# Optimization experiments

Hardware: AMD Instinct MI355X
Metric: run time of the kernel (lower is better)

Reference implementation:

```python
import jax, jax.numpy as jnp
import numpy as np

B, T = 64, 256
STOCH, DETER = 1024, 4096
D = 512          # attention_dim == embed_dim == heads*dim_head
H, HD = 8, 64    # heads, dim_head
FF = 2 * D       # feedforward hidden
L = 2            # transformer layers
NT = 255         # embedding rows (len(targets))
OUT = 255        # np.prod(shape)
SCALE = HD ** -0.5
EPS = 1e-5


def _ln(x, g, b):
    m = jnp.mean(x, axis=-1, keepdims=True)
    v = jnp.mean((x - m) ** 2, axis=-1, keepdims=True)
    return (x - m) * jax.lax.rsqrt(v + EPS) * g + b


def setup_inputs() -> dict:
    key = jax.random.key(0)
    ks = jax.random.split(key, 32)
    r = lambda i, shp, s=0.02: (jax.random.normal(ks[i], shp, dtype=jnp.float32) * s)
    inp = {
        'stoch': jax.random.normal(ks[0], (B, T, STOCH), dtype=jnp.float32),
        'deter': jax.random.normal(ks[1], (B, T, DETER), dtype=jnp.float32),
        'targets_array': jax.random.randint(ks[2], (B, T), 0, NT),
        'emb': r(3, (NT, D), 1.0),
        'Ws': r(4, (D, STOCH)), 'bs': jnp.zeros((D,), jnp.float32),
        'Wd': r(5, (D, DETER)), 'bd': jnp.zeros((D,), jnp.float32),
        # per-layer stacked params [L, ...]
        'ln1_g': jnp.ones((L, D), jnp.float32), 'ln1_b': jnp.zeros((L, D), jnp.float32),
        'Wqkv': r(6, (L, 3 * H * HD, D)),
        'Wout': r(7, (L, D, H * HD)), 'bout': jnp.zeros((L, D), jnp.float32),
        'ln2_g': jnp.ones((L, D), jnp.float32), 'ln2_b': jnp.zeros((L, D), jnp.float32),
        'W1': r(8, (L, FF, D)), 'b1': jnp.zeros((L, FF), jnp.float32),
        'W2': r(9, (L, D, FF)), 'b2': jnp.zeros((L, D), jnp.float32),
        'W1b': r(10, (L, FF, D)), 'b1b': jnp.zeros((L, FF), jnp.float32),
        'W2b': r(11, (L, D, FF)), 'b2b': jnp.zeros((L, D), jnp.float32),
        'Wm': r(12, (OUT, D)), 'bm': jnp.zeros((OUT,), jnp.float32),
    }
    return inp


def _forward(stoch, deter, targets_array, emb, Ws, bs, Wd, bd,
             ln1_g, ln1_b, Wqkv, Wout, bout, ln2_g, ln2_b,
             W1, b1, W2, b2, W1b, b1b, W2b, b2b, Wm, bm):
    N = B * T
    s = stoch.reshape(N, STOCH)
    d = deter.reshape(N, DETER)
    tg = targets_array.reshape(N)
    tok1 = (s @ Ws.T + bs)[:, None, :]   # [N,1,D]
    tok2 = (d @ Wd.T + bd)[:, None, :]
    x = jnp.concatenate([tok1, tok2], axis=1)   # [N,2,D]
    q2 = emb[tg][:, None, :]                    # [N,1,D]

    for l in range(L):
        # PreNorm -> Attention (residuals connect to the normalized inputs,
        # exactly as in the original code)
        xn = _ln(x, ln1_g[l], ln1_b[l])
        qn = _ln(q2, ln1_g[l], ln1_b[l])
        qkv = xn @ Wqkv[l].T                            # [N,2,3*H*HD]
        q, k, v = jnp.split(qkv, 3, axis=-1)
        q = q.reshape(N, 2, H, HD).transpose(0, 2, 1, 3)   # [N,H,2,HD]
        k = k.reshape(N, 2, H, HD).transpose(0, 2, 1, 3)
        v = v.reshape(N, 2, H, HD).transpose(0, 2, 1, 3)
        qq2 = qn.reshape(N, 1, H, HD).transpose(0, 2, 1, 3)  # [N,H,1,HD]
        dots = jnp.einsum('nhqd,nhkd->nhqk', q, k) * SCALE
        dots2 = jnp.einsum('nhqd,nhkd->nhqk', qq2, k) * SCALE
        attn = jax.nn.log_softmax(dots, axis=-1)    # LogSoftmax attention!
        attn2 = jax.nn.log_softmax(dots2, axis=-1)
        out = jnp.einsum('nhqk,nhkd->nhqd', attn, v).transpose(0, 2, 1, 3).reshape(N, 2, H * HD)
        qout = jnp.einsum('nhqk,nhkd->nhqd', attn2, v).transpose(0, 2, 1, 3).reshape(N, 1, H * HD)
        x = out @ Wout[l].T + bout[l] + xn   # to_out on self stream only
        q2 = qout + qn                        # cross stream has NO projection

        # PreNorm -> FeedForward (dual streams, separate MLPs, exact GELU)
        xn = _ln(x, ln2_g[l], ln2_b[l])
        qn = _ln(q2, ln2_g[l], ln2_b[l])
        x = jax.nn.gelu(xn @ W1[l].T + b1[l], approximate=False) @ W2[l].T + b2[l] + xn
        q2 = jax.nn.gelu(qn @ W1b[l].T + b1b[l], approximate=False) @ W2b[l].T + b2b[l] + qn

    out = q2.reshape(B, T, D)
    mean = out @ Wm.T + bm   # [B,T,OUT]
    return mean


def reference(stoch, deter, targets_array, emb, Ws, bs, Wd, bd,
              ln1_g, ln1_b, Wqkv, Wout, bout, ln2_g, ln2_b,
              W1, b1, W2, b2, W1b, b1b, W2b, b2b, Wm, bm):
    return _forward(stoch, deter, targets_array, emb, Ws, bs, Wd, bd,
                    ln1_g, ln1_b, Wqkv, Wout, bout, ln2_g, ln2_b,
                    W1, b1, W2, b2, W1b, b1b, W2b, b2b, Wm, bm)
```

## Files before the change

kernel.cpp:

```cpp
#include <hip/hip_runtime.h>
#include <cstdint>
#include <cstddef>


#define NTOK   16384
#define TWO_N  32768
#define DMODEL 512
#define HEADS  8
#define HDIM   64
#define FFDIM  1024
#define KSTOCH 1024
#define KDETER 4096
#define QKVD   1536
#define NOUT   255

typedef short bf16x8 __attribute__((ext_vector_type(8)));
typedef float f32x4  __attribute__((ext_vector_type(4)));

__device__ inline unsigned short bfbits(float f) {
  union { float f; unsigned u; } x; x.f = f;
  unsigned r = x.u + 0x7fffu + ((x.u >> 16) & 1u);
  return (unsigned short)(r >> 16);
}
__device__ inline float bf2f(unsigned short s) {
  union { unsigned u; float f; } x; x.u = ((unsigned)s) << 16;
  return x.f;
}
__device__ inline float wave_sum(float v) {
  #pragma unroll
  for (int o = 32; o > 0; o >>= 1) v += __shfl_xor(v, o);
  return v;
}

struct CvtEnt { const float* src; unsigned short* dst; int n4; int ntot4; };
struct CvtArgs { CvtEnt e[11]; };

__global__ __launch_bounds__(256) void cvt_kernel(CvtArgs args) {
  CvtEnt ent = args.e[blockIdx.y];
  int stride = gridDim.x * 256;
  for (int i = blockIdx.x * 256 + threadIdx.x; i < ent.ntot4; i += stride) {
    float4 v;
    if (i < ent.n4) v = ((const float4*)ent.src)[i];
    else            v = make_float4(0.f, 0.f, 0.f, 0.f);
    ushort4 o;
    o.x = bfbits(v.x); o.y = bfbits(v.y); o.z = bfbits(v.z); o.w = bfbits(v.w);
    ((ushort4*)ent.dst)[i] = o;
  }
}

__global__ __launch_bounds__(128) void gather_kernel(
    const float* __restrict__ emb, const int* __restrict__ tg,
    float* __restrict__ q2) {
  int n = blockIdx.x;
  int row = tg[n];
  ((float4*)(q2 + (size_t)n * DMODEL))[threadIdx.x] =
      ((const float4*)(emb + (size_t)row * DMODEL))[threadIdx.x];
}

__global__ __launch_bounds__(256) void ln2_kernel(
    const float* __restrict__ xs, const float* __restrict__ qs,
    const float* __restrict__ g, const float* __restrict__ b,
    unsigned short* __restrict__ xb, unsigned short* __restrict__ qb) {
  int w = threadIdx.x >> 6, l = threadIdx.x & 63;
  int row = blockIdx.x * 4 + w;
  const float* src;
  unsigned short* dst;
  if (row < TWO_N) {
    src = xs + (size_t)row * DMODEL;
    dst = xb + (size_t)row * DMODEL;
  } else {
    int r2 = row - TWO_N;
    src = qs + (size_t)r2 * DMODEL;
    dst = qb + (size_t)r2 * DMODEL;
  }
  float4 v0 = ((const float4*)src)[l];
  float4 v1 = ((const float4*)src)[l + 64];
  float s  = v0.x + v0.y + v0.z + v0.w + v1.x + v1.y + v1.z + v1.w;
  float ss = v0.x*v0.x + v0.y*v0.y + v0.z*v0.z + v0.w*v0.w
           + v1.x*v1.x + v1.y*v1.y + v1.z*v1.z + v1.w*v1.w;
  s = wave_sum(s); ss = wave_sum(ss);
  float mean = s * (1.f / DMODEL);
  float var  = ss * (1.f / DMODEL) - mean * mean;
  float r = rsqrtf(var + 1e-5f);

  float4 g0 = ((const float4*)g)[l],      b0 = ((const float4*)b)[l];
  float4 g1 = ((const float4*)g)[l + 64], b1 = ((const float4*)b)[l + 64];
  ushort4 p0, p1;
  p0.x = bfbits((v0.x - mean) * r * g0.x + b0.x);
  p0.y = bfbits((v0.y - mean) * r * g0.y + b0.y);
  p0.z = bfbits((v0.z - mean) * r * g0.z + b0.z);
  p0.w = bfbits((v0.w - mean) * r * g0.w + b0.w);
  p1.x = bfbits((v1.x - mean) * r * g1.x + b1.x);
  p1.y = bfbits((v1.y - mean) * r * g1.y + b1.y);
  p1.z = bfbits((v1.z - mean) * r * g1.z + b1.z);
  p1.w = bfbits((v1.w - mean) * r * g1.w + b1.w);
  ((ushort4*)dst)[l] = p0; ((ushort4*)dst)[l + 64] = p1;
}

__global__ __launch_bounds__(256) void attn_kernel(
    const unsigned short* __restrict__ qkv, const unsigned short* __restrict__ qnb,
    float* __restrict__ q2, unsigned short* __restrict__ attnout) {
  int w = threadIdx.x >> 6, l = threadIdx.x & 63;
  int idx = blockIdx.x * 4 + w;
  int n = idx >> 3, h = idx & 7;
  const unsigned short* r0 = qkv + (size_t)(2 * n) * QKVD + h * HDIM + l;
  float q0 = bf2f(r0[0]),     k0 = bf2f(r0[512]),      v0 = bf2f(r0[1024]);
  float q1 = bf2f(r0[QKVD]),  k1 = bf2f(r0[QKVD+512]), v1 = bf2f(r0[QKVD+1024]);
  size_t qoff = (size_t)n * DMODEL + h * HDIM + l;
  float qq = bf2f(qnb[qoff]);

  float d00 = q0*k0, d01 = q0*k1, d10 = q1*k0, d11 = q1*k1, e0 = qq*k0, e1 = qq*k1;
  #pragma unroll
  for (int o = 32; o > 0; o >>= 1) {
    d00 += __shfl_xor(d00, o); d01 += __shfl_xor(d01, o);
    d10 += __shfl_xor(d10, o); d11 += __shfl_xor(d11, o);
    e0  += __shfl_xor(e0, o);  e1  += __shfl_xor(e1, o);
  }
  const float SC = 0.125f;
  d00 *= SC; d01 *= SC; d10 *= SC; d11 *= SC; e0 *= SC; e1 *= SC;
  auto lsm2 = [](float& a, float& b) {
    float m = fmaxf(a, b);
    float lse = m + logf(expf(a - m) + expf(b - m));
    a -= lse; b -= lse;
  };
  lsm2(d00, d01); lsm2(d10, d11); lsm2(e0, e1);

  float o0 = d00 * v0 + d01 * v1;
  float o1 = d10 * v0 + d11 * v1;
  float oq = e0 * v0 + e1 * v1;
  attnout[(size_t)(2 * n)     * DMODEL + h * HDIM + l] = bfbits(o0);
  attnout[(size_t)(2 * n + 1) * DMODEL + h * HDIM + l] = bfbits(o1);
  q2[qoff] = oq + qq;
}

template <bool GELU>
__global__ __launch_bounds__(256, 3) void gemm_kernel(
    const unsigned short* __restrict__ A, const unsigned short* __restrict__ B,
    const float* __restrict__ bias, const unsigned short* __restrict__ res,
    float* __restrict__ Cf, unsigned short* __restrict__ Cb,
    int M, int Nvalid, int K, int ldc, int ldcb, int ldres, int ntn) {
  __shared__ short lsA[128 * 64];
  __shared__ short lsB[128 * 64];
  int nwg = gridDim.x;
  int q8 = nwg >> 3, r8 = nwg & 7;
  int xcd = blockIdx.x & 7, lin = blockIdx.x >> 3;
  int bid = (xcd < r8 ? xcd * (q8 + 1) : r8 * (q8 + 1) + (xcd - r8) * q8) + lin;
  int tm = bid / ntn, tn = bid % ntn;
  int tid = threadIdx.x;
  int w = tid >> 6, l = tid & 63;
  int wr = w >> 1, wc = w & 1;

  int srow = w * 32 + (l >> 3);
  int scol = (l & 7) * 8;
  const unsigned short* ga = A + (size_t)(tm * 128 + srow) * K + scol;
  const unsigned short* gb = B + (size_t)(tn * 128 + srow) * K + scol;
  short* la = lsA + w * 2048;
  short* lb = lsB + w * 2048;

  f32x4 acc[4][4] = {};

  for (int k0 = 0; k0 < K; k0 += 64) {
    #pragma unroll
    for (int r = 0; r < 4; ++r) {
      __builtin_amdgcn_global_load_lds(
          (const __attribute__((address_space(1))) void*)(ga + k0 + (size_t)r * 8 * K),
          (__attribute__((address_space(3))) void*)(la + r * 512), 16, 0, 0);
      __builtin_amdgcn_global_load_lds(
          (const __attribute__((address_space(1))) void*)(gb + k0 + (size_t)r * 8 * K),
          (__attribute__((address_space(3))) void*)(lb + r * 512), 16, 0, 0);
    }
    __syncthreads();
    #pragma unroll
    for (int kk = 0; kk < 2; ++kk) {
      bf16x8 af[4], bfr[4];
      #pragma unroll
      for (int i = 0; i < 4; ++i)
        af[i] = *(const bf16x8*)(lsA + (wr * 64 + i * 16 + (l & 15)) * 64 +
                                 kk * 32 + (l >> 4) * 8);
      #pragma unroll
      for (int i = 0; i < 4; ++i)
        bfr[i] = *(const bf16x8*)(lsB + (wc * 64 + i * 16 + (l & 15)) * 64 +
                                  kk * 32 + (l >> 4) * 8);
      #pragma unroll
      for (int mi = 0; mi < 4; ++mi)
        #pragma unroll
        for (int ni = 0; ni < 4; ++ni)
          acc[mi][ni] = __builtin_amdgcn_mfma_f32_16x16x32_bf16(
              af[mi], bfr[ni], acc[mi][ni], 0, 0, 0);
    }
    __syncthreads();
  }

  int lr = l >> 4, lc = l & 15;
  #pragma unroll
  for (int mi = 0; mi < 4; ++mi) {
    #pragma unroll
    for (int ni = 0; ni < 4; ++ni) {
      int gn = tn * 128 + wc * 64 + ni * 16 + lc;
      bool okn = gn < Nvalid;
      float bv = (bias != nullptr && okn) ? bias[gn] : 0.f;
      f32x4 a = acc[mi][ni];
      #pragma unroll
      for (int j = 0; j < 4; ++j) {
        int gm = tm * 128 + wr * 64 + mi * 16 + lr * 4 + j;
        float v = a[j] + bv;
        if (GELU) v = 0.5f * v * (1.f + erff(v * 0.70710678118654752f));
        if (okn) {
          if (res) v += bf2f(res[(size_t)gm * ldres + gn]);
          if (Cf) Cf[(size_t)gm * ldc + gn] = v;
          if (Cb) Cb[(size_t)gm * ldcb + gn] = bfbits(v);
        }
      }
    }
  }
}

extern "C" void kernel_launch(void* const* d_in, const int* in_sizes, int n_in,
                              void* d_out, int out_size, void* d_ws, size_t ws_size,
                              hipStream_t stream) {
  const float* stoch = (const float*)d_in[0];
  const float* deter = (const float*)d_in[1];
  const int*   tg    = (const int*)d_in[2];
  const float* emb   = (const float*)d_in[3];
  const float* Ws    = (const float*)d_in[4];
  const float* bs    = (const float*)d_in[5];
  const float* Wd    = (const float*)d_in[6];
  const float* bd    = (const float*)d_in[7];
  const float* ln1g  = (const float*)d_in[8];
  const float* ln1b  = (const float*)d_in[9];
  const float* Wqkv  = (const float*)d_in[10];
  const float* Wout  = (const float*)d_in[11];
  const float* bout  = (const float*)d_in[12];
  const float* ln2g  = (const float*)d_in[13];
  const float* ln2b  = (const float*)d_in[14];
  const float* W1    = (const float*)d_in[15];
  const float* b1    = (const float*)d_in[16];
  const float* W2    = (const float*)d_in[17];
  const float* b2    = (const float*)d_in[18];
  const float* W1b   = (const float*)d_in[19];
  const float* b1b   = (const float*)d_in[20];
  const float* W2b   = (const float*)d_in[21];
  const float* b2b   = (const float*)d_in[22];
  const float* Wm    = (const float*)d_in[23];
  const float* bm    = (const float*)d_in[24];
  float* out = (float*)d_out;

  char* p = (char*)d_ws;
  size_t off = 0;
  auto alloc = [&](size_t bytes) {
    void* r = p + off;
    off += (bytes + 255) & ~(size_t)255;
    return r;
  };
  unsigned short* s_bf = (unsigned short*)alloc((size_t)NTOK * KSTOCH * 2);
  unsigned short* d_bf = (unsigned short*)alloc((size_t)NTOK * KDETER * 2);
  float* x    = (float*)alloc((size_t)TWO_N * DMODEL * 4);
  float* q2   = (float*)alloc((size_t)NTOK * DMODEL * 4);
  unsigned short* xnb  = (unsigned short*)alloc((size_t)TWO_N * DMODEL * 2);
  unsigned short* qnb  = (unsigned short*)alloc((size_t)NTOK * DMODEL * 2);
  unsigned short* qkvb = (unsigned short*)alloc((size_t)TWO_N * QKVD * 2);
  unsigned short* Wsb   = (unsigned short*)alloc((size_t)DMODEL * KSTOCH * 2);
  unsigned short* Wdb   = (unsigned short*)alloc((size_t)DMODEL * KDETER * 2);
  unsigned short* Wqkvb = (unsigned short*)alloc((size_t)2 * QKVD * DMODEL * 2);
  unsigned short* Woutb = (unsigned short*)alloc((size_t)2 * DMODEL * DMODEL * 2);
  unsigned short* W1bf  = (unsigned short*)alloc((size_t)2 * FFDIM * DMODEL * 2);
  unsigned short* W2bf  = (unsigned short*)alloc((size_t)2 * DMODEL * FFDIM * 2);
  unsigned short* W1bbf = (unsigned short*)alloc((size_t)2 * FFDIM * DMODEL * 2);
  unsigned short* W2bbf = (unsigned short*)alloc((size_t)2 * DMODEL * FFDIM * 2);
  unsigned short* Wmb   = (unsigned short*)alloc((size_t)256 * DMODEL * 2);
  unsigned short* attnout = s_bf;
  unsigned short* q2b     = d_bf;
  unsigned short* hb      = qkvb;
  unsigned short* hqb     = qkvb + (size_t)TWO_N * FFDIM;

  CvtArgs ca;
  ca.e[0]  = { stoch, s_bf,  NTOK * KSTOCH / 4,  NTOK * KSTOCH / 4 };
  ca.e[1]  = { deter, d_bf,  NTOK * KDETER / 4,  NTOK * KDETER / 4 };
  ca.e[2]  = { Ws,    Wsb,   DMODEL * KSTOCH / 4, DMODEL * KSTOCH / 4 };
  ca.e[3]  = { Wd,    Wdb,   DMODEL * KDETER / 4, DMODEL * KDETER / 4 };
  ca.e[4]  = { Wqkv,  Wqkvb, 2 * QKVD * DMODEL / 4, 2 * QKVD * DMODEL / 4 };
  ca.e[5]  = { Wout,  Woutb, 2 * DMODEL * DMODEL / 4, 2 * DMODEL * DMODEL / 4 };
  ca.e[6]  = { W1,    W1bf,  2 * FFDIM * DMODEL / 4, 2 * FFDIM * DMODEL / 4 };
  ca.e[7]  = { W2,    W2bf,  2 * DMODEL * FFDIM / 4, 2 * DMODEL * FFDIM / 4 };
  ca.e[8]  = { W1b,   W1bbf, 2 * FFDIM * DMODEL / 4, 2 * FFDIM * DMODEL / 4 };
  ca.e[9]  = { W2b,   W2bbf, 2 * DMODEL * FFDIM / 4, 2 * DMODEL * FFDIM / 4 };
  ca.e[10] = { Wm,    Wmb,   NOUT * DMODEL / 4,   256 * DMODEL / 4 };
  cvt_kernel<<<dim3(1024, 11), 256, 0, stream>>>(ca);

  gemm_kernel<false><<<128 * 4, 256, 0, stream>>>(
      s_bf, Wsb, bs, nullptr, x, nullptr, NTOK, DMODEL, KSTOCH, 2 * DMODEL, 0, 0, 4);
  gemm_kernel<false><<<128 * 4, 256, 0, stream>>>(
      d_bf, Wdb, bd, nullptr, x + DMODEL, nullptr, NTOK, DMODEL, KDETER, 2 * DMODEL, 0, 0, 4);

  gather_kernel<<<NTOK, 128, 0, stream>>>(emb, tg, q2);

  const int LN_GRID = (TWO_N + NTOK) / 4;
  for (int l = 0; l < 2; ++l) {
    ln2_kernel<<<LN_GRID, 256, 0, stream>>>(x, q2, ln1g + 512 * l, ln1b + 512 * l, xnb, qnb);
    gemm_kernel<false><<<256 * 12, 256, 0, stream>>>(
        xnb, Wqkvb + (size_t)l * QKVD * DMODEL, nullptr, nullptr, nullptr, qkvb,
        TWO_N, QKVD, DMODEL, 0, QKVD, 0, 12);
    attn_kernel<<<NTOK * HEADS / 4, 256, 0, stream>>>(qkvb, qnb, q2, attnout);
    gemm_kernel<false><<<256 * 4, 256, 0, stream>>>(
        attnout, Woutb + (size_t)l * DMODEL * DMODEL, bout + 512 * l, xnb, x, nullptr,
        TWO_N, DMODEL, DMODEL, DMODEL, 0, DMODEL, 4);
    ln2_kernel<<<LN_GRID, 256, 0, stream>>>(x, q2, ln2g + 512 * l, ln2b + 512 * l, xnb, qnb);
    gemm_kernel<true><<<256 * 8, 256, 0, stream>>>(
        xnb, W1bf + (size_t)l * FFDIM * DMODEL, b1 + 1024 * l, nullptr, nullptr, hb,
        TWO_N, FFDIM, DMODEL, 0, FFDIM, 0, 8);
    gemm_kernel<false><<<256 * 4, 256, 0, stream>>>(
        hb, W2bf + (size_t)l * DMODEL * FFDIM, b2 + 512 * l, xnb, x, nullptr,
        TWO_N, DMODEL, FFDIM, DMODEL, 0, DMODEL, 4);
    gemm_kernel<true><<<128 * 8, 256, 0, stream>>>(
        qnb, W1bbf + (size_t)l * FFDIM * DMODEL, b1b + 1024 * l, nullptr, nullptr, hqb,
        NTOK, FFDIM, DMODEL, 0, FFDIM, 0, 8);
    gemm_kernel<false><<<128 * 4, 256, 0, stream>>>(
        hqb, W2bbf + (size_t)l * DMODEL * FFDIM, b2b + 512 * l, qnb, q2, q2b,
        NTOK, DMODEL, FFDIM, DMODEL, DMODEL, DMODEL, 4);
  }

  gemm_kernel<false><<<128 * 2, 256, 0, stream>>>(
      q2b, Wmb, bm, nullptr, out, nullptr, NTOK, NOUT, DMODEL, NOUT, 0, 0, 2);

  (void)in_sizes; (void)n_in; (void)out_size; (void)ws_size;
}
```

Before: 1.810 ms.

## Fuse fp32-to-bf16 activation conversion into input projection GEMMs; store residual stream as bf16

Removes the separate conversion pass over the large stoch and deter activations. The input-projection GEMMs now load fp32 A tiles directly, convert them in registers and write bf16 into LDS. The self-stream residual x is also stored as bf16 instead of fp32, which halves its traffic in the layernorm and GEMM epilogues. In exchange the fused GEMMs lose the async global-to-LDS path for A and run with lower occupancy. Keeping the residual in bf16 also reduces its precision.

```diff
diff --git a/kernel.cpp b/kernel.cpp
--- a/kernel.cpp
+++ b/kernel.cpp
@@ -33,7 +33,7 @@
 }
 
 struct CvtEnt { const float* src; unsigned short* dst; int n4; int ntot4; };
-struct CvtArgs { CvtEnt e[11]; };
+struct CvtArgs { CvtEnt e[9]; };
 
 __global__ __launch_bounds__(256) void cvt_kernel(CvtArgs args) {
   CvtEnt ent = args.e[blockIdx.y];
@@ -58,43 +58,45 @@
 }
 
 __global__ __launch_bounds__(256) void ln2_kernel(
-    const float* __restrict__ xs, const float* __restrict__ qs,
+    const unsigned short* __restrict__ xs, const float* __restrict__ qs,
     const float* __restrict__ g, const float* __restrict__ b,
     unsigned short* __restrict__ xb, unsigned short* __restrict__ qb) {
   int w = threadIdx.x >> 6, l = threadIdx.x & 63;
   int row = blockIdx.x * 4 + w;
-  const float* src;
+  float e[8];
   unsigned short* dst;
   if (row < TWO_N) {
-    src = xs + (size_t)row * DMODEL;
+    const unsigned short* src = xs + (size_t)row * DMODEL;
+    bf16x8 v = ((const bf16x8*)src)[l];
+    #pragma unroll
+    for (int i = 0; i < 8; ++i) e[i] = bf2f((unsigned short)v[i]);
     dst = xb + (size_t)row * DMODEL;
   } else {
     int r2 = row - TWO_N;
-    src = qs + (size_t)r2 * DMODEL;
+    const float* src = qs + (size_t)r2 * DMODEL;
+    float4 v0 = ((const float4*)src)[2 * l];
+    float4 v1 = ((const float4*)src)[2 * l + 1];
+    e[0] = v0.x; e[1] = v0.y; e[2] = v0.z; e[3] = v0.w;
+    e[4] = v1.x; e[5] = v1.y; e[6] = v1.z; e[7] = v1.w;
     dst = qb + (size_t)r2 * DMODEL;
   }
-  float4 v0 = ((const float4*)src)[l];
-  float4 v1 = ((const float4*)src)[l + 64];
-  float s  = v0.x + v0.y + v0.z + v0.w + v1.x + v1.y + v1.z + v1.w;
-  float ss = v0.x*v0.x + v0.y*v0.y + v0.z*v0.z + v0.w*v0.w
-           + v1.x*v1.x + v1.y*v1.y + v1.z*v1.z + v1.w*v1.w;
+  float s = 0.f, ss = 0.f;
+  #pragma unroll
+  for (int i = 0; i < 8; ++i) { s += e[i]; ss += e[i] * e[i]; }
   s = wave_sum(s); ss = wave_sum(ss);
   float mean = s * (1.f / DMODEL);
   float var  = ss * (1.f / DMODEL) - mean * mean;
   float r = rsqrtf(var + 1e-5f);
 
-  float4 g0 = ((const float4*)g)[l],      b0 = ((const float4*)b)[l];
-  float4 g1 = ((const float4*)g)[l + 64], b1 = ((const float4*)b)[l + 64];
-  ushort4 p0, p1;
-  p0.x = bfbits((v0.x - mean) * r * g0.x + b0.x);
-  p0.y = bfbits((v0.y - mean) * r * g0.y + b0.y);
-  p0.z = bfbits((v0.z - mean) * r * g0.z + b0.z);
-  p0.w = bfbits((v0.w - mean) * r * g0.w + b0.w);
-  p1.x = bfbits((v1.x - mean) * r * g1.x + b1.x);
-  p1.y = bfbits((v1.y - mean) * r * g1.y + b1.y);
-  p1.z = bfbits((v1.z - mean) * r * g1.z + b1.z);
-  p1.w = bfbits((v1.w - mean) * r * g1.w + b1.w);
-  ((ushort4*)dst)[l] = p0; ((ushort4*)dst)[l + 64] = p1;
+  float4 g0 = ((const float4*)g)[2 * l], g1 = ((const float4*)g)[2 * l + 1];
+  float4 b0 = ((const float4*)b)[2 * l], b1 = ((const float4*)b)[2 * l + 1];
+  float gg[8] = {g0.x, g0.y, g0.z, g0.w, g1.x, g1.y, g1.z, g1.w};
+  float bb[8] = {b0.x, b0.y, b0.z, b0.w, b1.x, b1.y, b1.z, b1.w};
+  bf16x8 o;
+  #pragma unroll
+  for (int i = 0; i < 8; ++i)
+    o[i] = (short)bfbits((e[i] - mean) * r * gg[i] + bb[i]);
+  ((bf16x8*)dst)[l] = o;
 }
 
 __global__ __launch_bounds__(256) void attn_kernel(
@@ -133,9 +135,9 @@
   q2[qoff] = oq + qq;
 }
 
-template <bool GELU>
-__global__ __launch_bounds__(256, 3) void gemm_kernel(
-    const unsigned short* __restrict__ A, const unsigned short* __restrict__ B,
+template <bool GELU, bool AF32>
+__global__ __launch_bounds__(256, AF32 ? 2 : 3) void gemm_kernel(
+    const void* __restrict__ Av, const unsigned short* __restrict__ B,
     const float* __restrict__ bias, const unsigned short* __restrict__ res,
     float* __restrict__ Cf, unsigned short* __restrict__ Cb,
     int M, int Nvalid, int K, int ldc, int ldcb, int ldres, int ntn) {
@@ -152,19 +154,34 @@
 
   int srow = w * 32 + (l >> 3);
   int scol = (l & 7) * 8;
-  const unsigned short* ga = A + (size_t)(tm * 128 + srow) * K + scol;
+  const unsigned short* ga = nullptr;
+  const float* gaf = nullptr;
+  if (AF32) gaf = (const float*)Av + (size_t)(tm * 128 + srow) * K + scol;
+  else      ga  = (const unsigned short*)Av + (size_t)(tm * 128 + srow) * K + scol;
   const unsigned short* gb = B + (size_t)(tn * 128 + srow) * K + scol;
   short* la = lsA + w * 2048;
   short* lb = lsB + w * 2048;
+  short* lwa = lsA + w * 2048 + (l >> 3) * 64 + (l & 7) * 8;
 
   f32x4 acc[4][4] = {};
 
   for (int k0 = 0; k0 < K; k0 += 64) {
     #pragma unroll
     for (int r = 0; r < 4; ++r) {
-      __builtin_amdgcn_global_load_lds(
-          (const __attribute__((address_space(1))) void*)(ga + k0 + (size_t)r * 8 * K),
-          (__attribute__((address_space(3))) void*)(la + r * 512), 16, 0, 0);
+      if (AF32) {
+        float4 u0 = *(const float4*)(gaf + k0 + (size_t)r * 8 * K);
+        float4 u1 = *(const float4*)(gaf + k0 + (size_t)r * 8 * K + 4);
+        bf16x8 pk;
+        pk[0] = (short)bfbits(u0.x); pk[1] = (short)bfbits(u0.y);
+        pk[2] = (short)bfbits(u0.z); pk[3] = (short)bfbits(u0.w);
+        pk[4] = (short)bfbits(u1.x); pk[5] = (short)bfbits(u1.y);
+        pk[6] = (short)bfbits(u1.z); pk[7] = (short)bfbits(u1.w);
+        *(bf16x8*)(lwa + r * 512) = pk;
+      } else {
+        __builtin_amdgcn_global_load_lds(
+            (const __attribute__((address_space(1))) void*)(ga + k0 + (size_t)r * 8 * K),
+            (__attribute__((address_space(3))) void*)(la + r * 512), 16, 0, 0);
+      }
       __builtin_amdgcn_global_load_lds(
           (const __attribute__((address_space(1))) void*)(gb + k0 + (size_t)r * 8 * K),
           (__attribute__((address_space(3))) void*)(lb + r * 512), 16, 0, 0);
@@ -252,13 +269,13 @@
     off += (bytes + 255) & ~(size_t)255;
     return r;
   };
-  unsigned short* s_bf = (unsigned short*)alloc((size_t)NTOK * KSTOCH * 2);
-  unsigned short* d_bf = (unsigned short*)alloc((size_t)NTOK * KDETER * 2);
-  float* x    = (float*)alloc((size_t)TWO_N * DMODEL * 4);
-  float* q2   = (float*)alloc((size_t)NTOK * DMODEL * 4);
+  unsigned short* x    = (unsigned short*)alloc((size_t)TWO_N * DMODEL * 2);
+  float*          q2   = (float*)alloc((size_t)NTOK * DMODEL * 4);
   unsigned short* xnb  = (unsigned short*)alloc((size_t)TWO_N * DMODEL * 2);
   unsigned short* qnb  = (unsigned short*)alloc((size_t)NTOK * DMODEL * 2);
   unsigned short* qkvb = (unsigned short*)alloc((size_t)TWO_N * QKVD * 2);
+  unsigned short* attnout = (unsigned short*)alloc((size_t)TWO_N * DMODEL * 2);
+  unsigned short* q2b  = (unsigned short*)alloc((size_t)NTOK * DMODEL * 2);
   unsigned short* Wsb   = (unsigned short*)alloc((size_t)DMODEL * KSTOCH * 2);
   unsigned short* Wdb   = (unsigned short*)alloc((size_t)DMODEL * KDETER * 2);
   unsigned short* Wqkvb = (unsigned short*)alloc((size_t)2 * QKVD * DMODEL * 2);
@@ -268,58 +285,54 @@
   unsigned short* W1bbf = (unsigned short*)alloc((size_t)2 * FFDIM * DMODEL * 2);
   unsigned short* W2bbf = (unsigned short*)alloc((size_t)2 * DMODEL * FFDIM * 2);
   unsigned short* Wmb   = (unsigned short*)alloc((size_t)256 * DMODEL * 2);
-  unsigned short* attnout = s_bf;
-  unsigned short* q2b     = d_bf;
-  unsigned short* hb      = qkvb;
-  unsigned short* hqb     = qkvb + (size_t)TWO_N * FFDIM;
+  unsigned short* hb  = qkvb;
+  unsigned short* hqb = qkvb + (size_t)TWO_N * FFDIM;
 
   CvtArgs ca;
-  ca.e[0]  = { stoch, s_bf,  NTOK * KSTOCH / 4,  NTOK * KSTOCH / 4 };
-  ca.e[1]  = { deter, d_bf,  NTOK * KDETER / 4,  NTOK * KDETER / 4 };
-  ca.e[2]  = { Ws,    Wsb,   DMODEL * KSTOCH / 4, DMODEL * KSTOCH / 4 };
-  ca.e[3]  = { Wd,    Wdb,   DMODEL * KDETER / 4, DMODEL * KDETER / 4 };
-  ca.e[4]  = { Wqkv,  Wqkvb, 2 * QKVD * DMODEL / 4, 2 * QKVD * DMODEL / 4 };
-  ca.e[5]  = { Wout,  Woutb, 2 * DMODEL * DMODEL / 4, 2 * DMODEL * DMODEL / 4 };
-  ca.e[6]  = { W1,    W1bf,  2 * FFDIM * DMODEL / 4, 2 * FFDIM * DMODEL / 4 };
-  ca.e[7]  = { W2,    W2bf,  2 * DMODEL * FFDIM / 4, 2 * DMODEL * FFDIM / 4 };
-  ca.e[8]  = { W1b,   W1bbf, 2 * FFDIM * DMODEL / 4, 2 * FFDIM * DMODEL / 4 };
-  ca.e[9]  = { W2b,   W2bbf, 2 * DMODEL * FFDIM / 4, 2 * DMODEL * FFDIM / 4 };
-  ca.e[10] = { Wm,    Wmb,   NOUT * DMODEL / 4,   256 * DMODEL / 4 };
-  cvt_kernel<<<dim3(1024, 11), 256, 0, stream>>>(ca);
-
-  gemm_kernel<false><<<128 * 4, 256, 0, stream>>>(
-      s_bf, Wsb, bs, nullptr, x, nullptr, NTOK, DMODEL, KSTOCH, 2 * DMODEL, 0, 0, 4);
-  gemm_kernel<false><<<128 * 4, 256, 0, stream>>>(
-      d_bf, Wdb, bd, nullptr, x + DMODEL, nullptr, NTOK, DMODEL, KDETER, 2 * DMODEL, 0, 0, 4);
+  ca.e[0] = { Ws,   Wsb,   DMODEL * KSTOCH / 4, DMODEL * KSTOCH / 4 };
+  ca.e[1] = { Wd,   Wdb,   DMODEL * KDETER / 4, DMODEL * KDETER / 4 };
+  ca.e[2] = { Wqkv, Wqkvb, 2 * QKVD * DMODEL / 4, 2 * QKVD * DMODEL / 4 };
+  ca.e[3] = { Wout, Woutb, 2 * DMODEL * DMODEL / 4, 2 * DMODEL * DMODEL / 4 };
+  ca.e[4] = { W1,   W1bf,  2 * FFDIM * DMODEL / 4, 2 * FFDIM * DMODEL / 4 };
+  ca.e[5] = { W2,   W2bf,  2 * DMODEL * FFDIM / 4, 2 * DMODEL * FFDIM / 4 };
+  ca.e[6] = { W1b,  W1bbf, 2 * FFDIM * DMODEL / 4, 2 * FFDIM * DMODEL / 4 };
+  ca.e[7] = { W2b,  W2bbf, 2 * DMODEL * FFDIM / 4, 2 * DMODEL * FFDIM / 4 };
+  ca.e[8] = { Wm,   Wmb,   NOUT * DMODEL / 4,   256 * DMODEL / 4 };
+  cvt_kernel<<<dim3(256, 9), 256, 0, stream>>>(ca);
+
+  gemm_kernel<false, true><<<128 * 4, 256, 0, stream>>>(
+      stoch, Wsb, bs, nullptr, nullptr, x, NTOK, DMODEL, KSTOCH, 0, 2 * DMODEL, 0, 4);
+  gemm_kernel<false, true><<<128 * 4, 256, 0, stream>>>(
+      deter, Wdb, bd, nullptr, nullptr, x + DMODEL, NTOK, DMODEL, KDETER, 0, 2 * DMODEL, 0, 4);
 
   gather_kernel<<<NTOK, 128, 0, stream>>>(emb, tg, q2);
 
   const int LN_GRID = (TWO_N + NTOK) / 4;
   for (int l = 0; l < 2; ++l) {
     ln2_kernel<<<LN_GRID, 256, 0, stream>>>(x, q2, ln1g + 512 * l, ln1b + 512 * l, xnb, qnb);
-    gemm_kernel<false><<<256 * 12, 256, 0, stream>>>(
+    gemm_kernel<false, false><<<256 * 12, 256, 0, stream>>>(
         xnb, Wqkvb + (size_t)l * QKVD * DMODEL, nullptr, nullptr, nullptr, qkvb,
         TWO_N, QKVD, DMODEL, 0, QKVD, 0, 12);
     attn_kernel<<<NTOK * HEADS / 4, 256, 0, stream>>>(qkvb, qnb, q2, attnout);
-    gemm_kernel<false><<<256 * 4, 256, 0, stream>>>(
-        attnout, Woutb + (size_t)l * DMODEL * DMODEL, bout + 512 * l, xnb, x, nullptr,
-        TWO_N, DMODEL, DMODEL, DMODEL, 0, DMODEL, 4);
+    gemm_kernel<false, false><<<256 * 4, 256, 0, stream>>>(
+        attnout, Woutb + (size_t)l * DMODEL * DMODEL, bout + 512 * l, xnb, nullptr, x,
+        TWO_N, DMODEL, DMODEL, 0, DMODEL, DMODEL, 4);
     ln2_kernel<<<LN_GRID, 256, 0, stream>>>(x, q2, ln2g + 512 * l, ln2b + 512 * l, xnb, qnb);
-    gemm_kernel<true><<<256 * 8, 256, 0, stream>>>(
+    gemm_kernel<true, false><<<256 * 8, 256, 0, stream>>>(
         xnb, W1bf + (size_t)l * FFDIM * DMODEL, b1 + 1024 * l, nullptr, nullptr, hb,
         TWO_N, FFDIM, DMODEL, 0, FFDIM, 0, 8);
-    gemm_kernel<false><<<256 * 4, 256, 0, stream>>>(
-        hb, W2bf + (size_t)l * DMODEL * FFDIM, b2 + 512 * l, xnb, x, nullptr,
-        TWO_N, DMODEL, FFDIM, DMODEL, 0, DMODEL, 4);
-    gemm_kernel<true><<<128 * 8, 256, 0, stream>>>(
+    gemm_kernel<false, false><<<256 * 4, 256, 0, stream>>>(
+        hb, W2bf + (size_t)l * DMODEL * FFDIM, b2 + 512 * l, xnb, nullptr, x,
+        TWO_N, DMODEL, FFDIM, 0, DMODEL, DMODEL, 4);
+    gemm_kernel<true, false><<<128 * 8, 256, 0, stream>>>(
         qnb, W1bbf + (size_t)l * FFDIM * DMODEL, b1b + 1024 * l, nullptr, nullptr, hqb,
         NTOK, FFDIM, DMODEL, 0, FFDIM, 0, 8);
-    gemm_kernel<false><<<128 * 4, 256, 0, stream>>>(
+    gemm_kernel<false, false><<<128 * 4, 256, 0, stream>>>(
         hqb, W2bbf + (size_t)l * DMODEL * FFDIM, b2b + 512 * l, qnb, q2, q2b,
         NTOK, DMODEL, FFDIM, DMODEL, DMODEL, DMODEL, 4);
   }
 
-  gemm_kernel<false><<<128 * 2, 256, 0, stream>>>(
+  gemm_kernel<false, false><<<128 * 2, 256, 0, stream>>>(
       q2b, Wmb, bm, nullptr, out, nullptr, NTOK, NOUT, DMODEL, NOUT, 0, 0, 2);
 
   (void)in_sizes; (void)n_in; (void)out_size; (void)ws_size;
```

After: 1.794 ms. Within noise of the previous version (-0.9%).
